# Optimization experiments

Hardware: AMD Instinct MI355X
Metric: run time of the kernel (lower is better)

Reference implementation:

```python
import jax, jax.numpy as jnp
import numpy as np

HEAD_SIZE = 128
N_EMBD = 64
B, T = 8, 4096


def setup_inputs() -> dict:
    key = jax.random.key(0)
    k1, k2, k3, k4 = jax.random.split(key, 4)
    x = jax.random.normal(k1, (B, T, N_EMBD), dtype=jnp.float32)
    Wq = jax.random.normal(k2, (N_EMBD, HEAD_SIZE), dtype=jnp.float32) * (N_EMBD ** -0.5)
    Wk = jax.random.normal(k3, (N_EMBD, HEAD_SIZE), dtype=jnp.float32) * (N_EMBD ** -0.5)
    Wv = jax.random.normal(k4, (N_EMBD, HEAD_SIZE), dtype=jnp.float32) * (N_EMBD ** -0.5)
    return {"x": x, "Wq": Wq, "Wk": Wk, "Wv": Wv}


def reference(x, Wq, Wk, Wv):
    # x: [B, T, C]; single-head causal self-attention (nanoGPT Head)
    q = x @ Wq  # [B, T, H]
    k = x @ Wk  # [B, T, H]
    v = x @ Wv  # [B, T, H]
    scale = HEAD_SIZE ** -0.5
    scores = jnp.einsum("bth,bsh->bts", q, k) * scale  # [B, T, T]
    t = x.shape[1]
    causal = jnp.tril(jnp.ones((t, t), dtype=bool))  # [T, T]
    scores = jnp.where(causal[None, :, :], scores, jnp.float32(-jnp.inf))
    wei = jax.nn.softmax(scores, axis=-1)  # [B, T, T]; dropout p=0.0 -> identity
    out = jnp.einsum("bts,bsh->bth", wei, v)  # [B, T, H]
    return out
```

## Files before the change

kernel.cpp:

```cpp
#include <hip/hip_runtime.h>
#include <math.h>

#define BB 8
#define TT 4096
#define CC 64
#define HH 128
#define NTH 256
#define XSTR 72
#define WSTR 72
#define QSCALE ((float)(0.08838834764831845 * 1.4426950408889634))

typedef __attribute__((ext_vector_type(8)))  short short8;
typedef __attribute__((ext_vector_type(4)))  float floatx4;
typedef __attribute__((ext_vector_type(16))) float floatx16;

__device__ __forceinline__ unsigned short f2bf(float f) {
    union { float f; unsigned int u; } un; un.f = f;
    unsigned int r = un.u + 0x7FFF + ((un.u >> 16) & 1);
    return (unsigned short)(r >> 16);
}
__device__ __forceinline__ unsigned int pack2bf_fast(float a, float b) {
    union { float f; unsigned int u; } ua, ub; ua.f = a; ub.f = b;
    return __builtin_amdgcn_perm(ub.u + 0x8000u, ua.u + 0x8000u, 0x07060302u);
}
__device__ __forceinline__ float bflo(unsigned int u) {
    union { unsigned int u; float f; } x; x.u = u << 16; return x.f;
}
__device__ __forceinline__ float bfhi(unsigned int u) {
    union { unsigned int u; float f; } x; x.u = u & 0xffff0000u; return x.f;
}

__device__ __forceinline__ void gl_lds16(const void* g, void* l) {
    __builtin_amdgcn_global_load_lds(
        (const __attribute__((address_space(1))) unsigned int*)g,
        (__attribute__((address_space(3))) unsigned int*)l, 16, 0, 0);
}

__global__ __launch_bounds__(NTH) void wconv(
    const float* __restrict__ Wq, const float* __restrict__ Wk, const float* __restrict__ Wv,
    unsigned short* __restrict__ Wbf)
{
    const int id = blockIdx.x * NTH + threadIdx.x;
    const int mat = id >> 13;
    const int rem = id & 8191;
    const int h = rem & 127, c = rem >> 7;
    const float* W = mat == 0 ? Wq : (mat == 1 ? Wk : Wv);
    const float s = mat == 0 ? QSCALE : 1.0f;
    Wbf[(mat * HH + h) * WSTR + c] = f2bf(W[c * HH + h] * s);
}

__global__ __launch_bounds__(NTH) void qkv_mfma(
    const float* __restrict__ x, const unsigned short* __restrict__ Wbf,
    unsigned short* __restrict__ qb, unsigned short* __restrict__ Kf,
    unsigned short* __restrict__ Vf)
{
    __shared__ __align__(16) unsigned short xs[64 * XSTR];
    __shared__ __align__(16) unsigned short Wts[3 * HH * WSTR];

    const int tid  = threadIdx.x;
    const int w    = tid >> 6;
    const int lane = tid & 63;
    const int quad = lane >> 4;
    const int lr   = lane & 15;

    const int b    = blockIdx.x & 7;
    const int kblk = blockIdx.x >> 3;
    const int t0   = kblk * 64;
    const long long rbase = (long long)b * TT + t0;

    {
        const unsigned char* ws = (const unsigned char*)Wbf;
        unsigned char* wd = (unsigned char*)Wts;
#pragma unroll
        for (int it = 0; it < 14; ++it) {
            const int off = it * 4096 + tid * 16;
            if (off < 3 * HH * WSTR * 2)
                gl_lds16(ws + off, wd + off);
        }
    }
#pragma unroll
    for (int i = 0; i < 4; ++i) {
        const int idx = tid + i * NTH;
        const int r = idx >> 4, c4 = idx & 15;
        const float4 v = *(const float4*)(x + (rbase + r) * CC + c4 * 4);
        unsigned short tmp[4] = { f2bf(v.x), f2bf(v.y), f2bf(v.z), f2bf(v.w) };
        *(unsigned long long*)&xs[r * XSTR + c4 * 4] = *(unsigned long long*)tmp;
    }
    __syncthreads();

    const short8 bx0 = *(const short8*)&xs[(w * 16 + lr) * XSTR + quad * 8];
    const short8 bx1 = *(const short8*)&xs[(w * 16 + lr) * XSTR + 32 + quad * 8];

    {
        const unsigned short* Wrow = Wts;
#pragma unroll
        for (int ht = 0; ht < 8; ++ht) {
            const short8 aw0 = *(const short8*)(Wrow + (ht * 16 + lr) * WSTR + quad * 8);
            const short8 aw1 = *(const short8*)(Wrow + (ht * 16 + lr) * WSTR + 32 + quad * 8);
            floatx4 acc = (floatx4)0.f;
            acc = __builtin_amdgcn_mfma_f32_16x16x32_bf16(aw0, bx0, acc, 0, 0, 0);
            acc = __builtin_amdgcn_mfma_f32_16x16x32_bf16(aw1, bx1, acc, 0, 0, 0);
            ushort4 st = { f2bf(acc[0]), f2bf(acc[1]), f2bf(acc[2]), f2bf(acc[3]) };
            *(ushort4*)(qb + (rbase + w * 16 + lr) * HH + ht * 16 + quad * 4) = st;
        }
    }
    {
        const unsigned short* Wrow = Wts + 1 * HH * WSTR;
        const int khp = w >> 1;
        const int lqp = (w & 1) * 16 + lr;
        unsigned short* kdst = Kf + ((long long)((b * 64 + kblk) * 2 + khp)) * 4096
                             + ((quad >> 1) & 1) * 256 + lqp * 8 + (quad & 1) * 4;
#pragma unroll
        for (int ht = 0; ht < 8; ++ht) {
            const short8 aw0 = *(const short8*)(Wrow + (ht * 16 + lr) * WSTR + quad * 8);
            const short8 aw1 = *(const short8*)(Wrow + (ht * 16 + lr) * WSTR + 32 + quad * 8);
            floatx4 acc = (floatx4)0.f;
            acc = __builtin_amdgcn_mfma_f32_16x16x32_bf16(aw0, bx0, acc, 0, 0, 0);
            acc = __builtin_amdgcn_mfma_f32_16x16x32_bf16(aw1, bx1, acc, 0, 0, 0);
            ushort4 st = { f2bf(acc[0]), f2bf(acc[1]), f2bf(acc[2]), f2bf(acc[3]) };
            *(ushort4*)(kdst + ht * 512) = st;
        }
    }
    {
        const unsigned short* Wrow = Wts + 2 * HH * WSTR;
        const int khv = w >> 1, ksv = w & 1, lsv = (quad >> 1) & 1;
        unsigned short* vdst = Vf + (long long)(b * 64 + kblk) * 8192 + khv * 4096
                             + ksv * 512 + lsv * 256 + (quad & 1) * 4;
#pragma unroll
        for (int htp = 0; htp < 8; ++htp) {
            const short8 bw0 = *(const short8*)(Wrow + (htp * 16 + lr) * WSTR + quad * 8);
            const short8 bw1 = *(const short8*)(Wrow + (htp * 16 + lr) * WSTR + 32 + quad * 8);
            floatx4 acc = (floatx4)0.f;
            acc = __builtin_amdgcn_mfma_f32_16x16x32_bf16(bx0, bw0, acc, 0, 0, 0);
            acc = __builtin_amdgcn_mfma_f32_16x16x32_bf16(bx1, bw1, acc, 0, 0, 0);
            ushort4 st = { f2bf(acc[0]), f2bf(acc[1]), f2bf(acc[2]), f2bf(acc[3]) };
            *(ushort4*)(vdst + (htp >> 1) * 1024 + ((htp & 1) * 16 + lr) * 8) = st;
        }
    }
}

__device__ __forceinline__ void dma_tile32(
    const unsigned char* __restrict__ Kj, const unsigned char* __restrict__ Vj,
    unsigned char* buf, int w, int lane)
{
    const unsigned char* src;
    unsigned char* dst;
    if (w < 2) { src = Kj + w * 4096 + lane * 16;        dst = buf + w * 4096; }
    else       { src = Vj + (w - 2) * 4096 + lane * 16;  dst = buf + 8192 + (w - 2) * 4096; }
#pragma unroll
    for (int i = 0; i < 4; ++i)
        gl_lds16(src + i * 1024, dst + i * 1024);
}

__global__ __launch_bounds__(NTH, 3) void flash_splitk(
    const unsigned short* __restrict__ qb,
    const unsigned short* __restrict__ Kf,
    const unsigned short* __restrict__ Vf,
    unsigned short* __restrict__ Ob, float* __restrict__ Lb)
{
    __shared__ __align__(16) unsigned char KV[2][16384];

    const int tid  = threadIdx.x;
    const int w    = tid >> 6;
    const int lane = tid & 63;
    const int lq   = lane & 31;
    const int ls   = lane >> 5;

    const int id = blockIdx.x;
    const int b  = id & 7;
    const int c  = (id >> 3) & 3;
    const int qt = 31 - (id >> 5);
    const int len = qt + 1;
    const int lo  = c * len;
    const int hi  = lo + qt;

    const int q0 = qt * 128;
    const long long baset = (long long)b * TT;
    const unsigned char* Kbase = (const unsigned char*)Kf + (long long)b * 128 * 8192;
    const unsigned char* Vbase = (const unsigned char*)Vf + (long long)b * 128 * 8192;

    dma_tile32(Kbase + (long long)lo * 8192, Vbase + (long long)lo * 8192, KV[0], w, lane);

    short8 aq[8];
    {
        const unsigned short* qrp = qb + (baset + q0 + w * 32 + lq) * HH + ls * 8;
#pragma unroll
        for (int st = 0; st < 8; ++st)
            aq[st] = *(const short8*)(qrp + st * 16);
    }

    floatx16 o_acc[4];
#pragma unroll
    for (int ht = 0; ht < 4; ++ht) o_acc[ht] = (floatx16)0.f;
    float l_lane = 0.f;

    for (int j = lo; j <= hi; ++j) {
        const int cb = (j - lo) & 1;
        __syncthreads();
        if (j < hi)
            dma_tile32(Kbase + (long long)(j + 1) * 8192, Vbase + (long long)(j + 1) * 8192,
                       KV[cb ^ 1], w, lane);

        const int D = q0 + w * 32 - j * 32;
        if (D > -32) {
            const unsigned short* Kt = (const unsigned short*)&KV[cb][0];
            const unsigned short* Vt = (const unsigned short*)&KV[cb][8192];

            short8 kfr[8], vfr[8];
#pragma unroll
            for (int st = 0; st < 8; ++st)
                kfr[st] = *(const short8*)(Kt + st * 512 + lane * 8);
#pragma unroll
            for (int i = 0; i < 8; ++i)
                vfr[i] = *(const short8*)(Vt + (i >> 1) * 1024 + (i & 1) * 512 + lane * 8);

            floatx16 s_acc = (floatx16)0.f;
#pragma unroll
            for (int st = 0; st < 8; ++st)
                s_acc = __builtin_amdgcn_mfma_f32_32x32x16_bf16(kfr[st], aq[st], s_acc, 0, 0, 0);

            float p[16];
            if (D < 31) {
#pragma unroll
                for (int reg = 0; reg < 16; ++reg) {
                    const int kk = (reg & 3) + 8 * (reg >> 2) + 4 * ls;
                    p[reg] = (kk <= lq + D) ? __builtin_amdgcn_exp2f(s_acc[reg]) : 0.f;
                }
            } else {
#pragma unroll
                for (int reg = 0; reg < 16; ++reg)
                    p[reg] = __builtin_amdgcn_exp2f(s_acc[reg]);
            }
#pragma unroll
            for (int reg = 0; reg < 16; ++reg) l_lane += p[reg];

            unsigned int g[8], pg[8];
#pragma unroll
            for (int i = 0; i < 8; ++i) g[i] = pack2bf_fast(p[2 * i], p[2 * i + 1]);
#pragma unroll
            for (int i = 0; i < 8; ++i) pg[i] = __shfl_xor((int)g[i], 32);
            short8 bp[2];
#pragma unroll
            for (int ks = 0; ks < 2; ++ks) {
                union { short8 s; unsigned int u[4]; } fr;
                const int bs = ks * 4;
                if (ls == 0) {
                    fr.u[0] = g[bs];      fr.u[1] = g[bs + 1];
                    fr.u[2] = pg[bs];     fr.u[3] = pg[bs + 1];
                } else {
                    fr.u[0] = pg[bs + 2]; fr.u[1] = pg[bs + 3];
                    fr.u[2] = g[bs + 2];  fr.u[3] = g[bs + 3];
                }
                bp[ks] = fr.s;
            }

#pragma unroll
            for (int ht = 0; ht < 4; ++ht) {
                o_acc[ht] = __builtin_amdgcn_mfma_f32_32x32x16_bf16(vfr[ht * 2 + 0], bp[0], o_acc[ht], 0, 0, 0);
                o_acc[ht] = __builtin_amdgcn_mfma_f32_32x32x16_bf16(vfr[ht * 2 + 1], bp[1], o_acc[ht], 0, 0, 0);
            }
        }
    }

    const int pid = ((b * 32 + qt) << 2) + c;
    const float l2 = l_lane + __shfl_xor(l_lane, 32);
    if (lane < 32) Lb[pid * 128 + w * 32 + lq] = l2;

    unsigned short* od = Ob + (long long)pid * 16384 + (w * 32 + lq) * HH;
#pragma unroll
    for (int ht = 0; ht < 4; ++ht)
#pragma unroll
        for (int rg = 0; rg < 4; ++rg) {
            uint2 st;
            st.x = pack2bf_fast(o_acc[ht][rg * 4 + 0], o_acc[ht][rg * 4 + 1]);
            st.y = pack2bf_fast(o_acc[ht][rg * 4 + 2], o_acc[ht][rg * 4 + 3]);
            *(uint2*)(od + ht * 32 + rg * 8 + 4 * ls) = st;
        }
}

__global__ __launch_bounds__(NTH) void combine(
    const unsigned short* __restrict__ Ob, const float* __restrict__ Lb,
    float* __restrict__ out)
{
    const int id = blockIdx.x;
    const int b = id & 7;
    const int rest = id >> 3;
    const int qt = rest >> 3;
    const int eighth = rest & 7;
    const int tid = threadIdx.x;
    const int q = eighth * 16 + (tid >> 4);
    const int hg = tid & 15;
    const int pid0 = ((b * 32 + qt) << 2);

    float acc[8];
#pragma unroll
    for (int i = 0; i < 8; ++i) acc[i] = 0.f;
    float ltot = 0.f;

#pragma unroll
    for (int cc = 0; cc < 4; ++cc) {
        ltot += Lb[(pid0 + cc) * 128 + q];
        const uint4 d = *(const uint4*)(Ob + (long long)(pid0 + cc) * 16384 + q * HH + hg * 8);
        acc[0] += bflo(d.x); acc[1] += bfhi(d.x);
        acc[2] += bflo(d.y); acc[3] += bfhi(d.y);
        acc[4] += bflo(d.z); acc[5] += bfhi(d.z);
        acc[6] += bflo(d.w); acc[7] += bfhi(d.w);
    }
    const float inv = 1.f / ltot;
    float* op = out + ((long long)b * TT + qt * 128 + q) * HH + hg * 8;
    float4 s0 = make_float4(acc[0] * inv, acc[1] * inv, acc[2] * inv, acc[3] * inv);
    float4 s1 = make_float4(acc[4] * inv, acc[5] * inv, acc[6] * inv, acc[7] * inv);
    *(float4*)(op) = s0;
    *(float4*)(op + 4) = s1;
}

extern "C" void kernel_launch(void* const* d_in, const int* in_sizes, int n_in,
                              void* d_out, int out_size, void* d_ws, size_t ws_size,
                              hipStream_t stream)
{
    const float* x  = (const float*)d_in[0];
    const float* Wq = (const float*)d_in[1];
    const float* Wk = (const float*)d_in[2];
    const float* Wv = (const float*)d_in[3];
    float* out = (float*)d_out;

    const long long n = (long long)BB * TT * HH;
    unsigned short* qb = (unsigned short*)d_ws;
    unsigned short* Kf = qb + n;
    unsigned short* Vf = Kf + n;
    unsigned short* Ob = Vf + n;
    float*          Lb = (float*)(Ob + (long long)1024 * 16384);
    unsigned short* Wbf = (unsigned short*)(Lb + 1024 * 128);

    wconv<<<96, NTH, 0, stream>>>(Wq, Wk, Wv, Wbf);
    qkv_mfma<<<BB * (TT / 64), NTH, 0, stream>>>(x, Wbf, qb, Kf, Vf);
    flash_splitk<<<1024, NTH, 0, stream>>>(qb, Kf, Vf, Ob, Lb);
    combine<<<BB * 32 * 8, NTH, 0, stream>>>(Ob, Lb, out);
}
```

Baseline: 137.2 us.

## Fuse split-K combine into flash kernel via last-arriving-block atomic counter

Removes the separate combine launch. Each flash block writes its partial output and row sums as before, then increments a per-tile atomic counter. The fourth block to arrive for a tile reduces all four partials and writes the final fp32 output, looping over 128 rows in 8 passes. Counters are zeroed in the weight-conversion kernel. This saves a launch and may reuse partials still in cache, but the last block per tile now does serial extra work. There is also no explicit memory fence before the atomic, so visibility of the other blocks' partials is a correctness risk.

```diff
diff --git a/kernel.cpp b/kernel.cpp
--- a/kernel.cpp
+++ b/kernel.cpp
@@ -38,9 +38,11 @@
 
 __global__ __launch_bounds__(NTH) void wconv(
     const float* __restrict__ Wq, const float* __restrict__ Wk, const float* __restrict__ Wv,
-    unsigned short* __restrict__ Wbf)
-{
-    const int id = blockIdx.x * NTH + threadIdx.x;
+    unsigned short* __restrict__ Wbf, int* __restrict__ Cnt)
+{
+    const int tid = threadIdx.x;
+    if (blockIdx.x == 0) Cnt[tid] = 0;
+    const int id = blockIdx.x * NTH + tid;
     const int mat = id >> 13;
     const int rem = id & 8191;
     const int h = rem & 127, c = rem >> 7;
@@ -156,9 +158,11 @@
     const unsigned short* __restrict__ qb,
     const unsigned short* __restrict__ Kf,
     const unsigned short* __restrict__ Vf,
-    unsigned short* __restrict__ Ob, float* __restrict__ Lb)
+    unsigned short* __restrict__ Ob, float* __restrict__ Lb,
+    int* __restrict__ Cnt, float* __restrict__ out)
 {
     __shared__ __align__(16) unsigned char KV[2][16384];
+    __shared__ int sArr;
 
     const int tid  = threadIdx.x;
     const int w    = tid >> 6;
@@ -262,7 +266,8 @@
         }
     }
 
-    const int pid = ((b * 32 + qt) << 2) + c;
+    const int tile = b * 32 + qt;
+    const int pid = (tile << 2) + c;
     const float l2 = l_lane + __shfl_xor(l_lane, 32);
     if (lane < 32) Lb[pid * 128 + w * 32 + lq] = l2;
 
@@ -276,42 +281,37 @@
             st.y = pack2bf_fast(o_acc[ht][rg * 4 + 2], o_acc[ht][rg * 4 + 3]);
             *(uint2*)(od + ht * 32 + rg * 8 + 4 * ls) = st;
         }
-}
-
-__global__ __launch_bounds__(NTH) void combine(
-    const unsigned short* __restrict__ Ob, const float* __restrict__ Lb,
-    float* __restrict__ out)
-{
-    const int id = blockIdx.x;
-    const int b = id & 7;
-    const int rest = id >> 3;
-    const int qt = rest >> 3;
-    const int eighth = rest & 7;
-    const int tid = threadIdx.x;
-    const int q = eighth * 16 + (tid >> 4);
-    const int hg = tid & 15;
-    const int pid0 = ((b * 32 + qt) << 2);
-
-    float acc[8];
-#pragma unroll
-    for (int i = 0; i < 8; ++i) acc[i] = 0.f;
-    float ltot = 0.f;
-
-#pragma unroll
-    for (int cc = 0; cc < 4; ++cc) {
-        ltot += Lb[(pid0 + cc) * 128 + q];
-        const uint4 d = *(const uint4*)(Ob + (long long)(pid0 + cc) * 16384 + q * HH + hg * 8);
-        acc[0] += bflo(d.x); acc[1] += bfhi(d.x);
-        acc[2] += bflo(d.y); acc[3] += bfhi(d.y);
-        acc[4] += bflo(d.z); acc[5] += bfhi(d.z);
-        acc[6] += bflo(d.w); acc[7] += bfhi(d.w);
-    }
-    const float inv = 1.f / ltot;
-    float* op = out + ((long long)b * TT + qt * 128 + q) * HH + hg * 8;
-    float4 s0 = make_float4(acc[0] * inv, acc[1] * inv, acc[2] * inv, acc[3] * inv);
-    float4 s1 = make_float4(acc[4] * inv, acc[5] * inv, acc[6] * inv, acc[7] * inv);
-    *(float4*)(op) = s0;
-    *(float4*)(op + 4) = s1;
+
+    __syncthreads();
+    if (tid == 0) sArr = atomicAdd(&Cnt[tile], 1);
+    __syncthreads();
+    if (sArr == 3) {
+        const int pid0 = tile << 2;
+        const int hg = tid & 15;
+#pragma unroll
+        for (int pass = 0; pass < 8; ++pass) {
+            const int q = pass * 16 + (tid >> 4);
+            float acc[8];
+#pragma unroll
+            for (int i = 0; i < 8; ++i) acc[i] = 0.f;
+            float ltot = 0.f;
+#pragma unroll
+            for (int cc = 0; cc < 4; ++cc) {
+                ltot += Lb[(pid0 + cc) * 128 + q];
+                const uint4 d = *(const uint4*)(Ob + (long long)(pid0 + cc) * 16384 + q * HH + hg * 8);
+                acc[0] += bflo(d.x); acc[1] += bfhi(d.x);
+                acc[2] += bflo(d.y); acc[3] += bfhi(d.y);
+                acc[4] += bflo(d.z); acc[5] += bfhi(d.z);
+                acc[6] += bflo(d.w); acc[7] += bfhi(d.w);
+            }
+            const float inv = 1.f / ltot;
+            float* op = out + (baset + q0 + q) * HH + hg * 8;
+            float4 s0 = make_float4(acc[0] * inv, acc[1] * inv, acc[2] * inv, acc[3] * inv);
+            float4 s1 = make_float4(acc[4] * inv, acc[5] * inv, acc[6] * inv, acc[7] * inv);
+            *(float4*)(op) = s0;
+            *(float4*)(op + 4) = s1;
+        }
+    }
 }
 
 extern "C" void kernel_launch(void* const* d_in, const int* in_sizes, int n_in,
@@ -331,9 +331,9 @@
     unsigned short* Ob = Vf + n;
     float*          Lb = (float*)(Ob + (long long)1024 * 16384);
     unsigned short* Wbf = (unsigned short*)(Lb + 1024 * 128);
-
-    wconv<<<96, NTH, 0, stream>>>(Wq, Wk, Wv, Wbf);
+    int*            Cnt = (int*)(Wbf + 3 * HH * WSTR);
+
+    wconv<<<96, NTH, 0, stream>>>(Wq, Wk, Wv, Wbf, Cnt);
     qkv_mfma<<<BB * (TT / 64), NTH, 0, stream>>>(x, Wbf, qb, Kf, Vf);
-    flash_splitk<<<1024, NTH, 0, stream>>>(qb, Kf, Vf, Ob, Lb);
-    combine<<<BB * 32 * 8, NTH, 0, stream>>>(Ob, Lb, out);
-}
+    flash_splitk<<<1024, NTH, 0, stream>>>(qb, Kf, Vf, Ob, Lb, Cnt, out);
+}
```

After: 140.5 us. +2.4%, slower.

## Split causal KV range into fixed 16-tile chunks instead of four equal splits

Applied to the files above, without the earlier changes.

Replaces the four-way split-K per query tile with a variable number of chunks, each covering at most 16 KV tiles of 32 keys. Work items are enumerated triangularly (144 per batch), so blocks carry roughly equal work instead of scaling with query-tile index. The combine kernel now loops over a variable chunk count with computed offsets. In exchange the grid grows to 1152 blocks, and the decode step uses a small while loop.

```diff
diff --git a/kernel.cpp b/kernel.cpp
--- a/kernel.cpp
+++ b/kernel.cpp
@@ -8,6 +8,7 @@
 #define NTH 256
 #define XSTR 72
 #define WSTR 72
+#define NCH 144
 #define QSCALE ((float)(0.08838834764831845 * 1.4426950408889634))
 
 typedef __attribute__((ext_vector_type(8)))  short short8;
@@ -168,11 +169,15 @@
 
     const int id = blockIdx.x;
     const int b  = id & 7;
-    const int c  = (id >> 3) & 3;
-    const int qt = 31 - (id >> 5);
-    const int len = qt + 1;
-    const int lo  = c * len;
-    const int hi  = lo + qt;
+    const int u  = id >> 3;
+    int a = 0;
+    while (u >= 2 * (a + 1) * (a + 2)) ++a;
+    const int v  = u - 2 * a * (a + 1);
+    const int qt = 4 * a + v / (a + 1);
+    const int ch = v % (a + 1);
+    const int ntile = 4 * qt + 4;
+    const int lo  = ch * 16;
+    const int hi  = min(lo + 15, ntile - 1);
 
     const int q0 = qt * 128;
     const long long baset = (long long)b * TT;
@@ -262,7 +267,7 @@
         }
     }
 
-    const int pid = ((b * 32 + qt) << 2) + c;
+    const int pid = b * NCH + u;
     const float l2 = l_lane + __shfl_xor(l_lane, 32);
     if (lane < 32) Lb[pid * 128 + w * 32 + lq] = l2;
 
@@ -290,15 +295,18 @@
     const int tid = threadIdx.x;
     const int q = eighth * 16 + (tid >> 4);
     const int hg = tid & 15;
-    const int pid0 = ((b * 32 + qt) << 2);
+
+    const int a = qt >> 2;
+    const int cnt = a + 1;
+    const int off = 2 * a * (a + 1) + (qt & 3) * (a + 1);
+    const int pid0 = b * NCH + off;
 
     float acc[8];
 #pragma unroll
     for (int i = 0; i < 8; ++i) acc[i] = 0.f;
     float ltot = 0.f;
 
-#pragma unroll
-    for (int cc = 0; cc < 4; ++cc) {
+    for (int cc = 0; cc < cnt; ++cc) {
         ltot += Lb[(pid0 + cc) * 128 + q];
         const uint4 d = *(const uint4*)(Ob + (long long)(pid0 + cc) * 16384 + q * HH + hg * 8);
         acc[0] += bflo(d.x); acc[1] += bfhi(d.x);
@@ -329,11 +337,11 @@
     unsigned short* Kf = qb + n;
     unsigned short* Vf = Kf + n;
     unsigned short* Ob = Vf + n;
-    float*          Lb = (float*)(Ob + (long long)1024 * 16384);
-    unsigned short* Wbf = (unsigned short*)(Lb + 1024 * 128);
+    float*          Lb = (float*)(Ob + (long long)(BB * NCH) * 16384);
+    unsigned short* Wbf = (unsigned short*)(Lb + BB * NCH * 128);
 
     wconv<<<96, NTH, 0, stream>>>(Wq, Wk, Wv, Wbf);
     qkv_mfma<<<BB * (TT / 64), NTH, 0, stream>>>(x, Wbf, qb, Kf, Vf);
-    flash_splitk<<<1024, NTH, 0, stream>>>(qb, Kf, Vf, Ob, Lb);
+    flash_splitk<<<BB * NCH, NTH, 0, stream>>>(qb, Kf, Vf, Ob, Lb);
     combine<<<BB * 32 * 8, NTH, 0, stream>>>(Ob, Lb, out);
 }
```

Measured after the change: 144.9 us. 1.06x slower.
